# Optimization experiments

Hardware: AMD Instinct MI355X
Metric: run time of the kernel (lower is better)

Reference implementation:

```python
import jax, jax.numpy as jnp
import numpy as np

N = 50000        # nodes
E = 1_600_000    # edges (avg degree 32)
D_IN = 128
HID = 256
D_OUT = 128      # must equal D_IN for the residual add


def setup_inputs() -> dict:
    key = jax.random.key(0)
    k0, k1, k2, k3 = jax.random.split(key, 4)
    x = jax.random.normal(k0, (N, D_IN), dtype=jnp.float32)
    edge_index = jax.random.randint(k1, (2, E), 0, N, dtype=jnp.int32)
    # GCNConv params (lin: Linear without bias in PyG, plus additive bias)
    W1 = jax.random.normal(k2, (D_IN, HID), dtype=jnp.float32) / np.sqrt(D_IN)
    b1 = jnp.zeros((HID,), jnp.float32)
    W2 = jax.random.normal(k3, (HID, D_OUT), dtype=jnp.float32) / np.sqrt(HID)
    b2 = jnp.zeros((D_OUT,), jnp.float32)
    return {"x": x, "edge_index": edge_index, "W1": W1, "b1": b1, "W2": W2, "b2": b2}


def _gcn_conv(x, src, dst, norm, W, b, n):
    # PyG GCNConv: transform, gather source features, scale by sym-norm, scatter-add to dst.
    h = x @ W                        # [n, d_out]
    msg = h[src] * norm[:, None]     # [E+n, d_out] gathered messages
    out = jax.ops.segment_sum(msg, dst, num_segments=n)
    return out + b


def reference(x, edge_index, W1, b1, W2, b2):
    n = x.shape[0]
    # add self loops (GCNConv default add_self_loops=True)
    loops = jnp.arange(n, dtype=edge_index.dtype)
    src = jnp.concatenate([edge_index[0], loops])
    dst = jnp.concatenate([edge_index[1], loops])
    # symmetric normalization D^{-1/2} (A+I) D^{-1/2}
    deg = jax.ops.segment_sum(jnp.ones_like(dst, dtype=x.dtype), dst, num_segments=n)
    dinv = jnp.where(deg > 0, jax.lax.rsqrt(deg), 0.0)
    norm = dinv[src] * dinv[dst]
    skip = x  # nn.Identity skip connection
    h = jax.nn.relu(_gcn_conv(x, src, dst, norm, W1, b1, n))
    out = _gcn_conv(h, src, dst, norm, W2, b2, n)
    # classification_layer treated as identity; original .double() cast kept in fp32
    return out + skip
```

## Files before the change

### kernel.cpp

```cpp
#include <hip/hip_runtime.h>

#define D_IN 128
#define HID 256
#define BKT_SHIFT 6
#define BKT_SIZE 64
#define BKT_CAP 3072
#define NBKT_MAX 1024
#define CHUNK 4096
#define PAD_SLACK 512
#define LSTR 264
#define ASTR 136

typedef __attribute__((ext_vector_type(8))) short short8;
typedef __attribute__((ext_vector_type(4))) float floatx4;
typedef __attribute__((ext_vector_type(4))) int intx4;

static __device__ __forceinline__ unsigned short f2b(float f) {
  unsigned u = __float_as_uint(f);
  unsigned r = (u + 0x7fffu + ((u >> 16) & 1u)) >> 16;
  return (unsigned short)r;
}

static __device__ __forceinline__ void unpack8(uint4 v, float* f) {
  f[0] = __uint_as_float(v.x << 16); f[1] = __uint_as_float(v.x & 0xffff0000u);
  f[2] = __uint_as_float(v.y << 16); f[3] = __uint_as_float(v.y & 0xffff0000u);
  f[4] = __uint_as_float(v.z << 16); f[5] = __uint_as_float(v.z & 0xffff0000u);
  f[6] = __uint_as_float(v.w << 16); f[7] = __uint_as_float(v.w & 0xffff0000u);
}

static __device__ __forceinline__ void acc_add(float* acc, uint4 v) {
  float g[8];
  unpack8(v, g);
#pragma unroll
  for (int d = 0; d < 8; ++d) acc[d] += g[d];
}

static __device__ __forceinline__ void gather_row(float* acc, const uint4* __restrict__ Hq,
                                                  const int* __restrict__ csr,
                                                  int2 se, int lane) {
  intx4 c0 = *(const intx4*)(csr + se.x);
  intx4 c1 = *(const intx4*)(csr + se.x + 4);
  for (int j = se.x; j < se.y; ) {
    const int jn = j + 8;
    const int jp = (jn < se.y) ? jn : se.x;
    intx4 n0 = *(const intx4*)(csr + jp);
    intx4 n1 = *(const intx4*)(csr + jp + 4);
    uint4 v0 = Hq[(size_t)c0.x * 16 + lane];
    uint4 v1 = Hq[(size_t)c0.y * 16 + lane];
    uint4 v2 = Hq[(size_t)c0.z * 16 + lane];
    uint4 v3 = Hq[(size_t)c0.w * 16 + lane];
    uint4 v4 = Hq[(size_t)c1.x * 16 + lane];
    uint4 v5 = Hq[(size_t)c1.y * 16 + lane];
    uint4 v6 = Hq[(size_t)c1.z * 16 + lane];
    uint4 v7 = Hq[(size_t)c1.w * 16 + lane];
    acc_add(acc, v0);
    acc_add(acc, v1);
    acc_add(acc, v2);
    acc_add(acc, v3);
    acc_add(acc, v4);
    acc_add(acc, v5);
    acc_add(acc, v6);
    acc_add(acc, v7);
    c0 = n0; c1 = n1; j = jn;
  }
}


__global__ __launch_bounds__(256) void fused_front_kernel(
    const int* __restrict__ src, const int* __restrict__ dst,
    int* __restrict__ bkt_cursor, int* __restrict__ ebuf, int E, int nbkt, int nchunk,
    const float* __restrict__ W1, unsigned short* __restrict__ Wt1,
    const float* __restrict__ W2, unsigned short* __restrict__ Wt2,
    float* __restrict__ dinv, unsigned short* __restrict__ xb,
    unsigned short* __restrict__ tb, int N) {
  const int bid = blockIdx.x;
  const int tid = threadIdx.x;
  if (bid < nchunk) {
    __shared__ int hist[NBKT_MAX];
    __shared__ int bbase[NBKT_MAX];
    for (int b = tid; b < nbkt; b += 256) hist[b] = 0;
    __syncthreads();
    const int base = bid * CHUNK;
    const int end = min(base + CHUNK, E);
    for (int e = base + tid; e < end; e += 256)
      atomicAdd(&hist[dst[e] >> BKT_SHIFT], 1);
    __syncthreads();
    for (int b = tid; b < nbkt; b += 256) {
      int c = hist[b];
      bbase[b] = c > 0 ? atomicAdd(&bkt_cursor[b], c) : 0;
      hist[b] = 0;
    }
    __syncthreads();
    for (int e = base + tid; e < end; e += 256) {
      int d = dst[e];
      int b = d >> BKT_SHIFT;
      int off = atomicAdd(&hist[b], 1);
      int rel = bbase[b] + off;
      if (rel < BKT_CAP)
        ebuf[b * BKT_CAP + rel] = (src[e] << BKT_SHIFT) | (d & (BKT_SIZE - 1));
    }
    return;
  }
  if (bid < nchunk + 128) {
    int e = (bid - nchunk) * 256 + tid;
    int k = e >> 8, n = e & 255;
    Wt1[(size_t)n * D_IN + k] = f2b(W1[e]);
  } else if (bid < nchunk + 256) {
    int e = (bid - nchunk - 128) * 256 + tid;
    int k = e >> 7, n = e & 127;
    Wt2[(size_t)n * HID + k] = f2b(W2[e]);
  } else {
    if (tid == 0) dinv[N] = 0.f;
    if (tid < 64)       ((unsigned*)(xb + (size_t)N * D_IN))[tid]      = 0u;
    else if (tid < 128) ((unsigned*)(tb + (size_t)N * D_IN))[tid - 64] = 0u;
  }
}


__global__ __launch_bounds__(256) void bucket_build_kernel(const int* __restrict__ ebuf,
                                                           const int* __restrict__ bkt_cursor,
                                                           const float4* __restrict__ x4,
                                                           unsigned short* __restrict__ xb,
                                                           float* __restrict__ dinv,
                                                           int2* __restrict__ rowse,
                                                           int* __restrict__ csr,
                                                           int N, int nbkt) {
  __shared__ int hist[BKT_SIZE];
  __shared__ int srs[BKT_SIZE];
  __shared__ float sdinv[BKT_SIZE];
  const int b = blockIdx.x;
  const int tid = threadIdx.x;
  const int node0 = b << BKT_SHIFT;
  const int nloc = min(BKT_SIZE, N - node0);
  const int ebeg = b * BKT_CAP;
  const int eend = ebeg + min(bkt_cursor[b], BKT_CAP);

  if (tid < BKT_SIZE) hist[tid] = 0;
  __syncthreads();
  for (int e = ebeg + tid; e < eend; e += 256)
    atomicAdd(&hist[ebuf[e] & (BKT_SIZE - 1)], 1);
  __syncthreads();

  if (tid < BKT_SIZE) {
    const int h = hist[tid];
    const int p = (h + 7) & ~7;
    int incl = p;
#pragma unroll
    for (int off = 1; off < 64; off <<= 1) {
      int t = __shfl_up(incl, off);
      if (tid >= off) incl += t;
    }
    const int ex = incl - p;
    float dv = rsqrtf((float)(h + 1));
    sdinv[tid] = dv;
    if (tid < nloc) {
      int st = b * (BKT_CAP + PAD_SLACK) + ex;
      dinv[node0 + tid] = dv;
      rowse[node0 + tid] = make_int2(st, st + p);
      srs[tid] = st;
    }
  }
  __syncthreads();
  if (tid < BKT_SIZE) hist[tid] = 0;
  __syncthreads();

  for (int e = ebeg + tid; e < eend; e += 256) {
    int u = ebuf[e];
    int l = u & (BKT_SIZE - 1);
    int pos = atomicAdd(&hist[l], 1);
    csr[srs[l] + pos] = u >> BKT_SHIFT;
  }
  __syncthreads();
  for (int l = tid; l < nloc; l += 256) {
    int deg = hist[l];
    int pp = (deg + 7) & ~7;
    int s0 = srs[l];
    for (int q = s0 + deg; q < s0 + pp; ++q) csr[q] = N;
  }

  for (int i = tid; i < nloc * 32; i += 256) {
    const int l = i >> 5;
    const float dv = sdinv[l];
    float4 v = x4[(size_t)(node0 + l) * 32 + (i & 31)];
    ushort4 o;
    o.x = f2b(v.x * dv); o.y = f2b(v.y * dv);
    o.z = f2b(v.z * dv); o.w = f2b(v.w * dv);
    *(ushort4*)(xb + (size_t)(node0 + l) * D_IN + (i & 31) * 4) = o;
  }
}


__global__ __launch_bounds__(512, 4) void agg1_gemm_kernel(
    const uint4* __restrict__ Hq, const int2* __restrict__ rowse,
    const int* __restrict__ csr, const float* __restrict__ dinv,
    const unsigned short* __restrict__ Wt1, const float* __restrict__ b1,
    const unsigned short* __restrict__ Wt2, unsigned short* __restrict__ T, int M) {
  __shared__ unsigned short as_[32][ASTR];
  __shared__ unsigned short hs[32][LSTR];
  const int tid = threadIdx.x;
  const int node0 = blockIdx.x * 32;

  {
    const int glane = tid & 15;
    const int lrow = tid >> 4;
    const int node = node0 + lrow;
    float acc[8] = {0.f, 0.f, 0.f, 0.f, 0.f, 0.f, 0.f, 0.f};
    float dv = 0.f;
    if (node < M) {
      dv = dinv[node];
      uint4 sv = Hq[(size_t)node * 16 + glane];
      unpack8(sv, acc);
      gather_row(acc, Hq, csr, rowse[node], glane);
    }
    uint4 o;
    o.x = (unsigned)f2b(acc[0] * dv) | ((unsigned)f2b(acc[1] * dv) << 16);
    o.y = (unsigned)f2b(acc[2] * dv) | ((unsigned)f2b(acc[3] * dv) << 16);
    o.z = (unsigned)f2b(acc[4] * dv) | ((unsigned)f2b(acc[5] * dv) << 16);
    o.w = (unsigned)f2b(acc[6] * dv) | ((unsigned)f2b(acc[7] * dv) << 16);
    *(uint4*)&as_[lrow][glane * 8] = o;
  }
  __syncthreads();

  const int wave = tid >> 6;
  const int lane = tid & 63;
  const int quad = lane >> 4;
  const int l16 = lane & 15;

  const short8* bp1 = (const short8*)(Wt1 + (size_t)(wave * 32 + l16) * D_IN + quad * 8);
  floatx4 acc1[2][2];
#pragma unroll
  for (int g = 0; g < 2; ++g)
#pragma unroll
    for (int t = 0; t < 2; ++t) acc1[g][t] = floatx4{0.f, 0.f, 0.f, 0.f};

#pragma unroll
  for (int kt = 0; kt < 4; ++kt) {
    short8 a0 = *(const short8*)&as_[0 * 16 + l16][kt * 32 + quad * 8];
    short8 a1 = *(const short8*)&as_[1 * 16 + l16][kt * 32 + quad * 8];
#pragma unroll
    for (int t = 0; t < 2; ++t) {
      short8 b = bp1[kt * 4 + t * 256];
      acc1[0][t] = __builtin_amdgcn_mfma_f32_16x16x32_bf16(a0, b, acc1[0][t], 0, 0, 0);
      acc1[1][t] = __builtin_amdgcn_mfma_f32_16x16x32_bf16(a1, b, acc1[1][t], 0, 0, 0);
    }
  }
#pragma unroll
  for (int t = 0; t < 2; ++t) {
    const float bv = b1[wave * 32 + t * 16 + l16];
#pragma unroll
    for (int g = 0; g < 2; ++g)
#pragma unroll
      for (int r = 0; r < 4; ++r) {
        float v = acc1[g][t][r] + bv;
        v = v > 0.f ? v : 0.f;
        hs[g * 16 + quad * 4 + r][wave * 32 + t * 16 + l16] = f2b(v);
      }
  }
  __syncthreads();

  const short8* bp2 = (const short8*)(Wt2 + (size_t)(wave * 16 + l16) * HID + quad * 8);
  floatx4 acc2[2];
#pragma unroll
  for (int g = 0; g < 2; ++g) acc2[g] = floatx4{0.f, 0.f, 0.f, 0.f};

#pragma unroll
  for (int kt = 0; kt < 8; ++kt) {
    short8 a0 = *(const short8*)&hs[0 * 16 + l16][kt * 32 + quad * 8];
    short8 a1 = *(const short8*)&hs[1 * 16 + l16][kt * 32 + quad * 8];
    short8 b = bp2[kt * 4];
    acc2[0] = __builtin_amdgcn_mfma_f32_16x16x32_bf16(a0, b, acc2[0], 0, 0, 0);
    acc2[1] = __builtin_amdgcn_mfma_f32_16x16x32_bf16(a1, b, acc2[1], 0, 0, 0);
  }
  __syncthreads();

#pragma unroll
  for (int g = 0; g < 2; ++g)
#pragma unroll
    for (int r = 0; r < 4; ++r) {
      int rr = node0 + g * 16 + quad * 4 + r;
      float dvr = dinv[rr < M ? rr : M];
      hs[g * 16 + quad * 4 + r][wave * 16 + l16] = f2b(acc2[g][r] * dvr);
    }
  __syncthreads();

  {
    const int r = tid >> 4;
    const int c = (tid & 15) * 8;
    const int row = node0 + r;
    uint4 v = *(const uint4*)&hs[r][c];
    if (row < M) *(uint4*)&T[(size_t)row * D_IN + c] = v;
  }
}


__global__ __launch_bounds__(256) void agg2_kernel(const uint4* __restrict__ Hq,
                                                   const int2* __restrict__ rowse,
                                                   const int* __restrict__ csr,
                                                   const float* __restrict__ dinv,
                                                   const float* __restrict__ skip,
                                                   const float* __restrict__ bias,
                                                   float* __restrict__ OUT, int n) {
  const int lane = threadIdx.x & 15;
  const int node = blockIdx.x * 16 + (threadIdx.x >> 4);
  if (node >= n) return;

  const float dv = dinv[node];
  float acc[8];
  {
    uint4 sv = Hq[(size_t)node * 16 + lane];
    unpack8(sv, acc);
  }
  gather_row(acc, Hq, csr, rowse[node], lane);

  const float* sp = skip + (size_t)node * 128 + lane * 8;
  const float* bp = bias + lane * 8;
  float4 s0 = *(const float4*)sp, s1 = *(const float4*)(sp + 4);
  float4 b0 = *(const float4*)bp, b1 = *(const float4*)(bp + 4);
  float* op = OUT + (size_t)node * 128 + lane * 8;
  *(float4*)op = make_float4(fmaf(acc[0], dv, s0.x + b0.x), fmaf(acc[1], dv, s0.y + b0.y),
                             fmaf(acc[2], dv, s0.z + b0.z), fmaf(acc[3], dv, s0.w + b0.w));
  *(float4*)(op + 4) = make_float4(fmaf(acc[4], dv, s1.x + b1.x), fmaf(acc[5], dv, s1.y + b1.y),
                                   fmaf(acc[6], dv, s1.z + b1.z), fmaf(acc[7], dv, s1.w + b1.w));
}


extern "C" void kernel_launch(void* const* d_in, const int* in_sizes, int n_in,
                              void* d_out, int out_size, void* d_ws, size_t ws_size,
                              hipStream_t stream) {
  const float* x  = (const float*)d_in[0];
  const int*   ei = (const int*)d_in[1];
  const float* W1 = (const float*)d_in[2];
  const float* b1 = (const float*)d_in[3];
  const float* W2 = (const float*)d_in[4];
  const float* b2 = (const float*)d_in[5];
  float* out = (float*)d_out;

  const int N = in_sizes[0] / D_IN;
  const int E = in_sizes[1] / 2;
  const int* srcA = ei;
  const int* dstA = ei + E;
  const int NBKT = (N + BKT_SIZE - 1) >> BKT_SHIFT;
  const int NCHUNK = (E + CHUNK - 1) / CHUNK;

  char* ws = (char*)d_ws;
  size_t off = 0;
  auto alloc = [&](size_t bytes) { void* p = ws + off; off = (off + bytes + 255) & ~(size_t)255; return p; };
  int*            bkt_cursor = (int*)           alloc((size_t)NBKT * 4);
  float*          dinv       = (float*)         alloc((size_t)(N + 1) * 4);
  int2*           rowse      = (int2*)          alloc((size_t)N * 8);
  int*            ebuf       = (int*)           alloc((size_t)NBKT * BKT_CAP * 4);
  int*            csr        = (int*)           alloc((size_t)NBKT * (BKT_CAP + PAD_SLACK) * 4);
  unsigned short* xb         = (unsigned short*)alloc((size_t)(N + 1) * D_IN * 2);
  unsigned short* tb         = (unsigned short*)alloc((size_t)(N + 1) * D_IN * 2);
  unsigned short* Wt1        = (unsigned short*)alloc((size_t)D_IN * HID * 2);
  unsigned short* Wt2        = (unsigned short*)alloc((size_t)D_IN * HID * 2);

  (void)hipMemsetAsync(bkt_cursor, 0, (size_t)NBKT * 4, stream);
  fused_front_kernel<<<NCHUNK + 256 + 1, 256, 0, stream>>>(
      srcA, dstA, bkt_cursor, ebuf, E, NBKT, NCHUNK,
      W1, Wt1, W2, Wt2, dinv, xb, tb, N);
  bucket_build_kernel<<<NBKT, 256, 0, stream>>>(ebuf, bkt_cursor, (const float4*)x,
                                                xb, dinv, rowse, csr, N, NBKT);
  agg1_gemm_kernel<<<(N + 31) / 32, 512, 0, stream>>>((const uint4*)xb, rowse, csr, dinv,
                                                      Wt1, b1, Wt2, tb, N);
  agg2_kernel<<<(N + 15) / 16, 256, 0, stream>>>((const uint4*)tb, rowse, csr,
                                                 dinv, x, b2, out, N);
}
```

Measured before the change: 261.5 us.

## Balance layer-1 edge gather across thread groups with shared-memory atomics

The layer-1 aggregation inside the fused agg+GEMM kernel no longer assigns one 16-lane group per destination row. It splits the block's 32 rows' edge chunks (8 edges each, from padded CSR) evenly across all 32 groups. Partial sums are accumulated in an fp32 shared buffer via LDS atomics, and that buffer is unioned with the bf16 hidden tile to keep LDS usage down. This removes load imbalance from skewed degrees, at the cost of LDS atomic traffic, an extra zeroing pass and extra barriers.

```diff
diff --git a/kernel.cpp b/kernel.cpp
--- a/kernel.cpp
+++ b/kernel.cpp
@@ -10,6 +10,7 @@
 #define PAD_SLACK 512
 #define LSTR 264
 #define ASTR 136
+#define FSTR 132
 
 typedef __attribute__((ext_vector_type(8))) short short8;
 typedef __attribute__((ext_vector_type(4))) float floatx4;
@@ -195,29 +196,92 @@
     const int* __restrict__ csr, const float* __restrict__ dinv,
     const unsigned short* __restrict__ Wt1, const float* __restrict__ b1,
     const unsigned short* __restrict__ Wt2, unsigned short* __restrict__ T, int M) {
+  __shared__ union {
+    float accf[32][FSTR];
+    unsigned short hs[32][LSTR];
+  } smu;
   __shared__ unsigned short as_[32][ASTR];
-  __shared__ unsigned short hs[32][LSTR];
+  __shared__ int srow[33];
   const int tid = threadIdx.x;
   const int node0 = blockIdx.x * 32;
+  const int nloc = min(32, M - node0);
 
   {
     const int glane = tid & 15;
-    const int lrow = tid >> 4;
-    const int node = node0 + lrow;
-    float acc[8] = {0.f, 0.f, 0.f, 0.f, 0.f, 0.f, 0.f, 0.f};
-    float dv = 0.f;
-    if (node < M) {
-      dv = dinv[node];
-      uint4 sv = Hq[(size_t)node * 16 + glane];
-      unpack8(sv, acc);
-      gather_row(acc, Hq, csr, rowse[node], glane);
-    }
-    uint4 o;
-    o.x = (unsigned)f2b(acc[0] * dv) | ((unsigned)f2b(acc[1] * dv) << 16);
-    o.y = (unsigned)f2b(acc[2] * dv) | ((unsigned)f2b(acc[3] * dv) << 16);
-    o.z = (unsigned)f2b(acc[4] * dv) | ((unsigned)f2b(acc[5] * dv) << 16);
-    o.w = (unsigned)f2b(acc[6] * dv) | ((unsigned)f2b(acc[7] * dv) << 16);
-    *(uint4*)&as_[lrow][glane * 8] = o;
+    const int grp = tid >> 4;
+    if (tid < nloc) {
+      int2 se = rowse[node0 + tid];
+      srow[tid] = se.x;
+      if (tid == nloc - 1) srow[nloc] = se.y;
+    }
+    for (int i = tid; i < 32 * FSTR; i += 512) (&smu.accf[0][0])[i] = 0.f;
+    __syncthreads();
+
+    const int s0 = srow[0];
+    const int C = (srow[nloc] - s0) >> 3;
+    const int c0 = (C * grp) >> 5, c1 = (C * (grp + 1)) >> 5;
+    if (c0 < c1) {
+      int r = 0;
+      int off = s0 + c0 * 8;
+      while (srow[r + 1] <= off) ++r;
+      float acc[8] = {0.f, 0.f, 0.f, 0.f, 0.f, 0.f, 0.f, 0.f};
+      for (int c = c0; c < c1; ++c) {
+        off = s0 + c * 8;
+        if (off >= srow[r + 1]) {
+#pragma unroll
+          for (int d = 0; d < 8; ++d) atomicAdd(&smu.accf[r][glane * 8 + d], acc[d]);
+#pragma unroll
+          for (int d = 0; d < 8; ++d) acc[d] = 0.f;
+          while (srow[r + 1] <= off) ++r;
+        }
+        intx4 i0 = *(const intx4*)(csr + off);
+        intx4 i1 = *(const intx4*)(csr + off + 4);
+        uint4 v0 = Hq[(size_t)i0.x * 16 + glane];
+        uint4 v1 = Hq[(size_t)i0.y * 16 + glane];
+        uint4 v2 = Hq[(size_t)i0.z * 16 + glane];
+        uint4 v3 = Hq[(size_t)i0.w * 16 + glane];
+        uint4 v4 = Hq[(size_t)i1.x * 16 + glane];
+        uint4 v5 = Hq[(size_t)i1.y * 16 + glane];
+        uint4 v6 = Hq[(size_t)i1.z * 16 + glane];
+        uint4 v7 = Hq[(size_t)i1.w * 16 + glane];
+        acc_add(acc, v0);
+        acc_add(acc, v1);
+        acc_add(acc, v2);
+        acc_add(acc, v3);
+        acc_add(acc, v4);
+        acc_add(acc, v5);
+        acc_add(acc, v6);
+        acc_add(acc, v7);
+      }
+#pragma unroll
+      for (int d = 0; d < 8; ++d) atomicAdd(&smu.accf[r][glane * 8 + d], acc[d]);
+    }
+    __syncthreads();
+
+    {
+      const int l = tid >> 4, cg = tid & 15;
+      float self[8] = {0.f, 0.f, 0.f, 0.f, 0.f, 0.f, 0.f, 0.f};
+      float dv = 0.f;
+      if (l < nloc) {
+        dv = dinv[node0 + l];
+        uint4 sv = Hq[(size_t)(node0 + l) * 16 + cg];
+        unpack8(sv, self);
+      }
+      uint4 o;
+      float a0 = (smu.accf[l][cg * 8 + 0] + self[0]) * dv;
+      float a1 = (smu.accf[l][cg * 8 + 1] + self[1]) * dv;
+      float a2 = (smu.accf[l][cg * 8 + 2] + self[2]) * dv;
+      float a3 = (smu.accf[l][cg * 8 + 3] + self[3]) * dv;
+      float a4 = (smu.accf[l][cg * 8 + 4] + self[4]) * dv;
+      float a5 = (smu.accf[l][cg * 8 + 5] + self[5]) * dv;
+      float a6 = (smu.accf[l][cg * 8 + 6] + self[6]) * dv;
+      float a7 = (smu.accf[l][cg * 8 + 7] + self[7]) * dv;
+      o.x = (unsigned)f2b(a0) | ((unsigned)f2b(a1) << 16);
+      o.y = (unsigned)f2b(a2) | ((unsigned)f2b(a3) << 16);
+      o.z = (unsigned)f2b(a4) | ((unsigned)f2b(a5) << 16);
+      o.w = (unsigned)f2b(a6) | ((unsigned)f2b(a7) << 16);
+      *(uint4*)&as_[l][cg * 8] = o;
+    }
   }
   __syncthreads();
 
@@ -253,7 +317,7 @@
       for (int r = 0; r < 4; ++r) {
         float v = acc1[g][t][r] + bv;
         v = v > 0.f ? v : 0.f;
-        hs[g * 16 + quad * 4 + r][wave * 32 + t * 16 + l16] = f2b(v);
+        smu.hs[g * 16 + quad * 4 + r][wave * 32 + t * 16 + l16] = f2b(v);
       }
   }
   __syncthreads();
@@ -265,8 +329,8 @@
 
 #pragma unroll
   for (int kt = 0; kt < 8; ++kt) {
-    short8 a0 = *(const short8*)&hs[0 * 16 + l16][kt * 32 + quad * 8];
-    short8 a1 = *(const short8*)&hs[1 * 16 + l16][kt * 32 + quad * 8];
+    short8 a0 = *(const short8*)&smu.hs[0 * 16 + l16][kt * 32 + quad * 8];
+    short8 a1 = *(const short8*)&smu.hs[1 * 16 + l16][kt * 32 + quad * 8];
     short8 b = bp2[kt * 4];
     acc2[0] = __builtin_amdgcn_mfma_f32_16x16x32_bf16(a0, b, acc2[0], 0, 0, 0);
     acc2[1] = __builtin_amdgcn_mfma_f32_16x16x32_bf16(a1, b, acc2[1], 0, 0, 0);
@@ -279,7 +343,7 @@
     for (int r = 0; r < 4; ++r) {
       int rr = node0 + g * 16 + quad * 4 + r;
       float dvr = dinv[rr < M ? rr : M];
-      hs[g * 16 + quad * 4 + r][wave * 16 + l16] = f2b(acc2[g][r] * dvr);
+      smu.hs[g * 16 + quad * 4 + r][wave * 16 + l16] = f2b(acc2[g][r] * dvr);
     }
   __syncthreads();
 
@@ -287,7 +351,7 @@
     const int r = tid >> 4;
     const int c = (tid & 15) * 8;
     const int row = node0 + r;
-    uint4 v = *(const uint4*)&hs[r][c];
+    uint4 v = *(const uint4*)&smu.hs[r][c];
     if (row < M) *(uint4*)&T[(size_t)row * D_IN + c] = v;
   }
 }
```

Measured after the change: 295.6 us. +13.0%, slower.
